# Optimization experiments

Hardware: AMD Instinct MI355X
Metric: run time of the kernel (lower is better)

The kernel has to match this reference:

```python
import jax, jax.numpy as jnp
import numpy as np

B, T, D = 1, 2048, 2048
H, HD = 32, 64
HEAD_COUNTS = np.array([8, 6, 4, 4, 6, 4])  # reasoning, creativity, curiosity, emotional, memory, meta
NEG = -1e9


def rope_tables(seq_len, dim, dtype):
    inv_freq = 1.0 / (10000.0 ** (jnp.arange(0, dim, 2, dtype=jnp.float32) / dim))
    t = jnp.arange(seq_len, dtype=jnp.float32)
    freqs = jnp.outer(t, inv_freq)            # [T, dim/2]
    emb = jnp.concatenate([freqs, freqs], -1) # [T, dim]
    return jnp.cos(emb).astype(dtype), jnp.sin(emb).astype(dtype)


def rotate_half(x):
    x1, x2 = jnp.split(x, 2, axis=-1)
    return jnp.concatenate([-x2, x1], axis=-1)


def setup_inputs() -> dict:
    key = jax.random.key(0)
    ks = jax.random.split(key, 8)
    x = jax.random.normal(ks[0], (B, T, D), jnp.float32)
    mask = jnp.tril(jnp.ones((T, T), jnp.int32))[None, None]  # causal [1,1,T,T]
    context_bias = jax.random.normal(ks[1], (B, T, T), jnp.float32) * 0.02
    mod_weights = jax.random.uniform(ks[2], (B, 6), jnp.float32, 0.5, 1.5)
    Wq = jax.random.normal(ks[3], (D, D), jnp.float32) * 0.02
    Wk = jax.random.normal(ks[4], (D, D), jnp.float32) * 0.02
    Wv = jax.random.normal(ks[5], (D, D), jnp.float32) * 0.02
    Wo = jax.random.normal(ks[6], (D, D), jnp.float32) * 0.02
    temp_scales = jnp.ones((H,), jnp.float32)
    return {"x": x, "mask": mask, "context_bias": context_bias,
            "mod_weights": mod_weights, "Wq": Wq, "Wk": Wk, "Wv": Wv,
            "Wo": Wo, "temp_scales": temp_scales}


def reference(x, mask, context_bias, mod_weights, Wq, Wk, Wv, Wo, temp_scales):
    b, t, d = x.shape
    # projections (torch Linear: y = x @ W.T)
    Q = (x @ Wq.T).reshape(b, t, H, HD).transpose(0, 2, 1, 3)  # [B,H,T,HD]
    K = (x @ Wk.T).reshape(b, t, H, HD).transpose(0, 2, 1, 3)
    V = (x @ Wv.T).reshape(b, t, H, HD).transpose(0, 2, 1, 3)
    cos, sin = rope_tables(t, HD, x.dtype)
    cos, sin = cos[None, None], sin[None, None]
    Q = Q * cos + rotate_half(Q) * sin
    K = K * cos + rotate_half(K) * sin
    scale = (HD ** -0.5) * temp_scales.reshape(1, H, 1, 1)
    attn = jnp.einsum('bhqd,bhkd->bhqk', Q, K) * scale
    attn = jnp.where(mask == 0, NEG, attn)
    attn = attn + context_bias[:, None]
    # per-head module reweight: expand [B,6] -> [B,H]
    w = jnp.repeat(mod_weights, np.asarray(HEAD_COUNTS), axis=1, total_repeat_length=H)
    attn = attn * w[:, :, None, None]
    attn = jax.nn.softmax(attn, axis=-1)
    out = jnp.einsum('bhqk,bhkd->bhqd', attn, V)
    out = out.transpose(0, 2, 1, 3).reshape(b, t, d)
    return out @ Wo.T
```

## Files before the change

kernel.cpp:

```cpp
#include <hip/hip_runtime.h>
#include <hip/hip_bf16.h>
#include <cstdint>
#include <cstddef>

typedef __bf16 bf16;
typedef bf16 bf16x4 __attribute__((ext_vector_type(4)));
typedef bf16 bf16x8 __attribute__((ext_vector_type(8)));
typedef float f32x4 __attribute__((ext_vector_type(4)));

#define MFMA_BF16(a,b,c) __builtin_amdgcn_mfma_f32_16x16x32_bf16((a),(b),(c),0,0,0)

typedef __attribute__((address_space(1))) const void gvoid;
typedef __attribute__((address_space(3))) void svoid;
__device__ __forceinline__ void gload16(const bf16* g, bf16* l){
  __builtin_amdgcn_global_load_lds((gvoid*)g, (svoid*)l, 16, 0, 0);
}

__device__ __forceinline__ int head_group(int h){
  return (h<8)?0:(h<14)?1:(h<18)?2:(h<22)?3:(h<28)?4:5;
}

struct CvtArgs { const float* src[5]; bf16* dst[5]; };
__global__ __launch_bounds__(256) void cvt5_kernel(CvtArgs a, int n){
  const int z = blockIdx.y;
  const float* __restrict__ in = a.src[z];
  bf16* __restrict__ out = a.dst[z];
  int i = (blockIdx.x*256 + threadIdx.x)*8;
  if (i >= n) return;
  const float4* p = (const float4*)(in + i);
  float4 va = p[0], vb = p[1];
  bf16x8 o;
  o[0]=(bf16)va.x; o[1]=(bf16)va.y; o[2]=(bf16)va.z; o[3]=(bf16)va.w;
  o[4]=(bf16)vb.x; o[5]=(bf16)vb.y; o[6]=(bf16)vb.z; o[7]=(bf16)vb.w;
  *(bf16x8*)(out+i) = o;
}

__global__ void rope_tab_kernel(float* __restrict__ cosT, float* __restrict__ sinT){
  int t = blockIdx.x, i = threadIdx.x;
  float invf = powf(10000.0f, -((float)i)/32.0f);
  float ang = (float)t * invf;
  cosT[t*32+i] = cosf(ang);
  sinT[t*32+i] = sinf(ang);
}

__device__ __forceinline__ void gemm_core(const bf16* __restrict__ A,
                                          const bf16* __restrict__ B,
                                          int row0, int col0,
                                          f32x4 (&acc)[4][4]){
  __shared__ bf16 As[128*32];
  __shared__ bf16 Bs[128*32];
  const int tid  = threadIdx.x;
  const int wave = tid>>6, lane = tid&63;
  const int l16  = lane&15, lg = lane>>4;
  const int wr   = wave>>1, wc = wave&1;

  const bf16* Ag0 = A + (size_t)(row0 + wave*32      + (lane>>2))*2048 + (lane&3)*8;
  const bf16* Ag1 = A + (size_t)(row0 + wave*32 + 16 + (lane>>2))*2048 + (lane&3)*8;
  const bf16* Bg0 = B + (size_t)(col0 + wave*32      + (lane>>2))*2048 + (lane&3)*8;
  const bf16* Bg1 = B + (size_t)(col0 + wave*32 + 16 + (lane>>2))*2048 + (lane&3)*8;
  bf16* AsB0 = As + (wave*32     )*32;
  bf16* AsB1 = As + (wave*32 + 16)*32;
  bf16* BsB0 = Bs + (wave*32     )*32;
  bf16* BsB1 = Bs + (wave*32 + 16)*32;

  #pragma unroll
  for (int m=0;m<4;++m)
    #pragma unroll
    for (int n=0;n<4;++n)
      #pragma unroll
      for (int r=0;r<4;++r) acc[m][n][r] = 0.f;

  for (int kt=0; kt<64; ++kt){
    const int ko = kt*32;
    gload16(Ag0 + ko, AsB0);
    gload16(Ag1 + ko, AsB1);
    gload16(Bg0 + ko, BsB0);
    gload16(Bg1 + ko, BsB1);
    __syncthreads();
    bf16x8 af[4], bfr[4];
    #pragma unroll
    for (int m=0;m<4;++m) af[m]  = *(const bf16x8*)&As[(wr*64+m*16+l16)*32 + lg*8];
    #pragma unroll
    for (int n=0;n<4;++n) bfr[n] = *(const bf16x8*)&Bs[(wc*64+n*16+l16)*32 + lg*8];
    #pragma unroll
    for (int m=0;m<4;++m)
      #pragma unroll
      for (int n=0;n<4;++n)
        acc[m][n] = MFMA_BF16(af[m], bfr[n], acc[m][n]);
    __syncthreads();
  }
}

__global__ __launch_bounds__(256) void gemm_qkv_kernel(
    const bf16* __restrict__ A,
    const bf16* __restrict__ B0, const bf16* __restrict__ B1, const bf16* __restrict__ B2,
    bf16* __restrict__ Qs, bf16* __restrict__ Ks, bf16* __restrict__ Vt,
    const float* __restrict__ cosT, const float* __restrict__ sinT,
    const float* __restrict__ mw, const float* __restrict__ ts){
  const int z = blockIdx.z;
  const bf16* B = (z==0)?B0:((z==1)?B1:B2);
  const int row0 = blockIdx.y*128, col0 = blockIdx.x*128;

  f32x4 acc[4][4];
  gemm_core(A, B, row0, col0, acc);

  const int tid  = threadIdx.x;
  const int wave = tid>>6, lane = tid&63;
  const int l16  = lane&15, lg = lane>>4;
  const int wr   = wave>>1, wc = wave&1;
  const int h    = (col0 + wc*64) >> 6;

  if (z == 2){
    #pragma unroll
    for (int n=0;n<4;++n){
      const int d = n*16 + l16;
      #pragma unroll
      for (int m=0;m<4;++m){
        const int t0 = row0 + wr*64 + m*16 + lg*4;
        bf16x4 v;
        #pragma unroll
        for (int r=0;r<4;++r) v[r] = (bf16)acc[m][n][r];
        *(bf16x4*)&Vt[((size_t)h*64 + d)*2048 + t0] = v;
      }
    }
  } else {
    const float sc = (z==0) ? 0.125f*ts[h]*mw[head_group(h)] : 1.0f;
    bf16* Out = (z==0) ? Qs : Ks;
    #pragma unroll
    for (int m=0;m<4;++m){
      #pragma unroll
      for (int r=0;r<4;++r){
        const int t = row0 + wr*64 + m*16 + lg*4 + r;
        const float* ct = cosT + t*32;
        const float* st = sinT + t*32;
        bf16* dst = Out + ((size_t)h*2048 + t)*64;
        #pragma unroll
        for (int n=0;n<2;++n){
          const int i = n*16 + l16;
          const float c = ct[i], s = st[i];
          const float a1 = acc[m][n][r], a2 = acc[m][n+2][r];
          dst[i]    = (bf16)((a1*c - a2*s)*sc);
          dst[i+32] = (bf16)((a2*c + a1*s)*sc);
        }
      }
    }
  }
}

__global__ __launch_bounds__(256) void gemm_out_kernel(
    const bf16* __restrict__ A, const bf16* __restrict__ B, float* __restrict__ C){
  const int row0 = blockIdx.y*128, col0 = blockIdx.x*128;
  f32x4 acc[4][4];
  gemm_core(A, B, row0, col0, acc);
  const int tid  = threadIdx.x;
  const int wave = tid>>6, lane = tid&63;
  const int l16  = lane&15, lg = lane>>4;
  const int wr   = wave>>1, wc = wave&1;
  #pragma unroll
  for (int m=0;m<4;++m)
    #pragma unroll
    for (int n=0;n<4;++n)
      #pragma unroll
      for (int r=0;r<4;++r){
        size_t idx = (size_t)(row0 + wr*64 + m*16 + lg*4 + r)*2048
                   + col0 + wc*64 + n*16 + l16;
        C[idx] = acc[m][n][r];
      }
}

__global__ __launch_bounds__(512) void attn_kernel(
    const bf16* __restrict__ Qs, const bf16* __restrict__ Ks,
    const bf16* __restrict__ Vt, const float* __restrict__ biasf,
    const float* __restrict__ mw, bf16* __restrict__ attout){
  const int n  = blockIdx.x;
  const int h  = ((n>>8)<<4) | ((n>>4)&15);
  const int qt = (n&256) ? (n&15) : 15-(n&15);
  const int tid = threadIdx.x, wid = tid>>6, lane = tid&63;
  const int l16 = lane&15, lg = lane>>4;
  const float w_h = mw[head_group(h)];
  const int qbase = qt*128 + wid*16;
  const int qg0 = qbase + lg*4;
  const int qtop = qbase + 15;
  const int nkt = 2*qt + 2;

  __shared__ bf16 Kl[2][4096];
  __shared__ bf16 Vl[2][4096];
  __shared__ bf16 plds[8][16][72];

  const int srow = tid>>3, ssub = tid&7;
  const bf16* Kg = Ks + (size_t)h*2048*64 + srow*64 + ssub*8;
  const bf16* Vg = Vt + ((size_t)h*64 + srow)*2048 + ssub*8;
  const int wsw = srow*64 + ((ssub ^ (srow&7))<<3);

  const bf16* Qp = Qs + ((size_t)h*2048 + qbase + l16)*64 + lg*8;
  bf16x8 qf0 = *(const bf16x8*)Qp;
  bf16x8 qf1 = *(const bf16x8*)(Qp + 32);

  const float* Bg = biasf + (size_t)qg0*2048;

  f32x4 O[4];
  float l[4] = {0.f,0.f,0.f,0.f};
  #pragma unroll
  for (int c=0;c<4;++c)
    #pragma unroll
    for (int r=0;r<4;++r) O[c][r] = 0.f;

  int rK0[4], rK1[4];
  #pragma unroll
  for (int c=0;c<4;++c){
    const int row = c*16 + l16;
    rK0[c] = row*64 + (((lg  ) ^ (row&7))<<3);
    rK1[c] = row*64 + (((4+lg) ^ (row&7))<<3);
  }

  {
    bf16x8 k0v = *(const bf16x8*)Kg;
    bf16x8 v0v = *(const bf16x8*)Vg;
    *(bf16x8*)&Kl[0][wsw] = k0v;
    *(bf16x8*)&Vl[0][wsw] = v0v;
  }
  __syncthreads();

  int cur = 0;
  for (int kt=0; kt<nkt; ++kt){
    const int k0 = kt*64;
    const bool more = (kt+1 < nkt);
    bf16x8 kA, vA;
    if (more){
      kA = *(const bf16x8*)(Kg + (size_t)(k0+64)*64);
      vA = *(const bf16x8*)(Vg + (k0+64));
    }

    if (k0 <= qtop){
      float bv[4][4];
      #pragma unroll
      for (int c=0;c<4;++c)
        #pragma unroll
        for (int r=0;r<4;++r)
          bv[c][r] = Bg[(size_t)r*2048 + k0 + c*16 + l16];

      f32x4 S[4];
      #pragma unroll
      for (int c=0;c<4;++c)
        #pragma unroll
        for (int r=0;r<4;++r) S[c][r] = 0.f;
      #pragma unroll
      for (int c=0;c<4;++c){
        bf16x8 kf0 = *(const bf16x8*)&Kl[cur][rK0[c]];
        bf16x8 kf1 = *(const bf16x8*)&Kl[cur][rK1[c]];
        S[c] = MFMA_BF16(qf0, kf0, S[c]);
        S[c] = MFMA_BF16(qf1, kf1, S[c]);
      }

      #pragma unroll
      for (int c=0;c<4;++c){
        const int kg = k0 + c*16 + l16;
        #pragma unroll
        for (int r=0;r<4;++r){
          float s = S[c][r] + w_h*bv[c][r];
          if (kg > qg0+r) s = -1e30f;
          const float p = __expf(s - 4.0f);
          S[c][r] = p; l[r] += p;
        }
      }

      #pragma unroll
      for (int c=0;c<4;++c)
        #pragma unroll
        for (int r=0;r<4;++r)
          plds[wid][lg*4+r][c*16+l16] = (bf16)S[c][r];
      bf16x8 pf0 = *(const bf16x8*)&plds[wid][l16][lg*8];
      bf16x8 pf1 = *(const bf16x8*)&plds[wid][l16][lg*8+32];

      #pragma unroll
      for (int c=0;c<4;++c){
        bf16x8 vf0 = *(const bf16x8*)&Vl[cur][rK0[c]];
        bf16x8 vf1 = *(const bf16x8*)&Vl[cur][rK1[c]];
        O[c] = MFMA_BF16(pf0, vf0, O[c]);
        O[c] = MFMA_BF16(pf1, vf1, O[c]);
      }
    }

    if (more){
      *(bf16x8*)&Kl[cur^1][wsw] = kA;
      *(bf16x8*)&Vl[cur^1][wsw] = vA;
    }
    __syncthreads();
    cur ^= (int)more;
  }

  #pragma unroll
  for (int r=0;r<4;++r){
    float v = l[r];
    v += __shfl_xor(v,1);
    v += __shfl_xor(v,2);
    v += __shfl_xor(v,4);
    v += __shfl_xor(v,8);
    l[r] = 1.0f / v;
  }
  #pragma unroll
  for (int c=0;c<4;++c)
    #pragma unroll
    for (int r=0;r<4;++r)
      attout[(size_t)(qg0+r)*2048 + h*64 + c*16 + l16] = (bf16)(O[c][r]*l[r]);
}

extern "C" void kernel_launch(void* const* d_in, const int* in_sizes, int n_in,
                              void* d_out, int out_size, void* d_ws, size_t ws_size,
                              hipStream_t stream){
  const float* x    = (const float*)d_in[0];
  const float* bias = (const float*)d_in[2];
  const float* mw   = (const float*)d_in[3];
  const float* Wq   = (const float*)d_in[4];
  const float* Wk   = (const float*)d_in[5];
  const float* Wv   = (const float*)d_in[6];
  const float* Wo   = (const float*)d_in[7];
  const float* ts   = (const float*)d_in[8];
  float* out = (float*)d_out;

  const size_t SZ = (size_t)2048*2048;
  bf16* base = (bf16*)d_ws;
  bf16* xb   = base;
  bf16* Wqb  = base + 1*SZ;
  bf16* Wkb  = base + 2*SZ;
  bf16* Wvb  = base + 3*SZ;
  bf16* Wob  = base + 4*SZ;
  bf16* Qsb  = base + 5*SZ;
  bf16* Ksb  = base + 6*SZ;
  bf16* Vtb  = base + 7*SZ;
  bf16* att  = base + 8*SZ;
  float* cosT = (float*)(base + 9*SZ);
  float* sinT = cosT + 2048*32;

  CvtArgs ca;
  ca.src[0]=x;  ca.src[1]=Wq;  ca.src[2]=Wk;  ca.src[3]=Wv;  ca.src[4]=Wo;
  ca.dst[0]=xb; ca.dst[1]=Wqb; ca.dst[2]=Wkb; ca.dst[3]=Wvb; ca.dst[4]=Wob;
  const int nb = (int)(SZ/8/256);
  cvt5_kernel<<<dim3(nb,5),256,0,stream>>>(ca, (int)SZ);
  rope_tab_kernel<<<2048,32,0,stream>>>(cosT, sinT);
  gemm_qkv_kernel<<<dim3(16,16,3),256,0,stream>>>(xb, Wqb,Wkb,Wvb,
                                                  Qsb,Ksb,Vtb, cosT,sinT, mw,ts);
  attn_kernel<<<512,512,0,stream>>>(Qsb,Ksb,Vtb,bias,mw,att);
  gemm_out_kernel<<<dim3(16,16),256,0,stream>>>(att, Wob, out);
}
```

Measured before the change: 181.6 us.

## Give each attention wave two query sub-tiles to reuse K/V fragments

The attention kernel moves from 8 waves of 16 query rows to 4 waves of 32 rows. Each K/V fragment read from LDS now feeds two MFMAs, halving the LDS fragment traffic per query row, and each thread now loads two 16-byte chunks of K/V per tile. It also seeds the S accumulators with the weighted bias, applies the causal mask only on diagonal tiles, and repacks the rope table kernel into 256-thread blocks. In exchange there are fewer waves per block and more registers per thread, which may lower occupancy and latency hiding.

```diff
diff --git a/kernel.cpp b/kernel.cpp
--- a/kernel.cpp
+++ b/kernel.cpp
@@ -35,8 +35,10 @@
   *(bf16x8*)(out+i) = o;
 }
 
-__global__ void rope_tab_kernel(float* __restrict__ cosT, float* __restrict__ sinT){
-  int t = blockIdx.x, i = threadIdx.x;
+__global__ __launch_bounds__(256) void rope_tab_kernel(float* __restrict__ cosT,
+                                                       float* __restrict__ sinT){
+  const int t = blockIdx.x*8 + (threadIdx.x>>5);
+  const int i = threadIdx.x&31;
   float invf = powf(10000.0f, -((float)i)/32.0f);
   float ang = (float)t * invf;
   cosT[t*32+i] = cosf(ang);
@@ -168,7 +170,7 @@
       }
 }
 
-__global__ __launch_bounds__(512) void attn_kernel(
+__global__ __launch_bounds__(256) void attn_kernel(
     const bf16* __restrict__ Qs, const bf16* __restrict__ Ks,
     const bf16* __restrict__ Vt, const float* __restrict__ biasf,
     const float* __restrict__ mw, bf16* __restrict__ attout){
@@ -178,32 +180,40 @@
   const int tid = threadIdx.x, wid = tid>>6, lane = tid&63;
   const int l16 = lane&15, lg = lane>>4;
   const float w_h = mw[head_group(h)];
-  const int qbase = qt*128 + wid*16;
-  const int qg0 = qbase + lg*4;
-  const int qtop = qbase + 15;
-  const int nkt = 2*qt + 2;
+  const int qw   = qt*128 + wid*32;
+  const int qtop = qw + 31;
+  const int nkt  = 2*qt + 2;
 
   __shared__ bf16 Kl[2][4096];
   __shared__ bf16 Vl[2][4096];
-  __shared__ bf16 plds[8][16][72];
-
-  const int srow = tid>>3, ssub = tid&7;
+  __shared__ bf16 plds[4][32][68];
+
+  const int srow = tid>>2, ssub = (tid&3)*2;
   const bf16* Kg = Ks + (size_t)h*2048*64 + srow*64 + ssub*8;
   const bf16* Vg = Vt + ((size_t)h*64 + srow)*2048 + ssub*8;
-  const int wsw = srow*64 + ((ssub ^ (srow&7))<<3);
-
-  const bf16* Qp = Qs + ((size_t)h*2048 + qbase + l16)*64 + lg*8;
-  bf16x8 qf0 = *(const bf16x8*)Qp;
-  bf16x8 qf1 = *(const bf16x8*)(Qp + 32);
-
-  const float* Bg = biasf + (size_t)qg0*2048;
-
-  f32x4 O[4];
-  float l[4] = {0.f,0.f,0.f,0.f};
-  #pragma unroll
-  for (int c=0;c<4;++c)
-    #pragma unroll
-    for (int r=0;r<4;++r) O[c][r] = 0.f;
+  const int wsw0 = srow*64 + (((ssub  ) ^ (srow&7))<<3);
+  const int wsw1 = srow*64 + (((ssub+1) ^ (srow&7))<<3);
+
+  bf16x8 qf[2][2];
+  #pragma unroll
+  for (int m=0;m<2;++m){
+    const bf16* Qp = Qs + ((size_t)h*2048 + qw + m*16 + l16)*64 + lg*8;
+    qf[m][0] = *(const bf16x8*)Qp;
+    qf[m][1] = *(const bf16x8*)(Qp + 32);
+  }
+
+  const float* Bg = biasf + (size_t)(qw + lg*4)*2048;
+
+  f32x4 O[2][4];
+  float l[2][4];
+  #pragma unroll
+  for (int m=0;m<2;++m)
+    #pragma unroll
+    for (int c=0;c<4;++c){
+      #pragma unroll
+      for (int r=0;r<4;++r) O[m][c][r] = 0.f;
+      l[m][c] = 0.f;
+    }
 
   int rK0[4], rK1[4];
   #pragma unroll
@@ -214,10 +224,12 @@
   }
 
   {
-    bf16x8 k0v = *(const bf16x8*)Kg;
-    bf16x8 v0v = *(const bf16x8*)Vg;
-    *(bf16x8*)&Kl[0][wsw] = k0v;
-    *(bf16x8*)&Vl[0][wsw] = v0v;
+    bf16x8 k0a = *(const bf16x8*)Kg;
+    bf16x8 k0b = *(const bf16x8*)(Kg + 8);
+    bf16x8 v0a = *(const bf16x8*)Vg;
+    bf16x8 v0b = *(const bf16x8*)(Vg + 8);
+    *(bf16x8*)&Kl[0][wsw0] = k0a;  *(bf16x8*)&Kl[0][wsw1] = k0b;
+    *(bf16x8*)&Vl[0][wsw0] = v0a;  *(bf16x8*)&Vl[0][wsw1] = v0b;
   }
   __syncthreads();
 
@@ -225,84 +237,114 @@
   for (int kt=0; kt<nkt; ++kt){
     const int k0 = kt*64;
     const bool more = (kt+1 < nkt);
-    bf16x8 kA, vA;
+    bf16x8 kA, kB, vA, vB;
     if (more){
-      kA = *(const bf16x8*)(Kg + (size_t)(k0+64)*64);
-      vA = *(const bf16x8*)(Vg + (k0+64));
+      const bf16* Kn = Kg + (size_t)(k0+64)*64;
+      const bf16* Vn = Vg + (k0+64);
+      kA = *(const bf16x8*)Kn;  kB = *(const bf16x8*)(Kn + 8);
+      vA = *(const bf16x8*)Vn;  vB = *(const bf16x8*)(Vn + 8);
     }
 
     if (k0 <= qtop){
-      float bv[4][4];
-      #pragma unroll
-      for (int c=0;c<4;++c)
-        #pragma unroll
-        for (int r=0;r<4;++r)
-          bv[c][r] = Bg[(size_t)r*2048 + k0 + c*16 + l16];
-
-      f32x4 S[4];
-      #pragma unroll
-      for (int c=0;c<4;++c)
-        #pragma unroll
-        for (int r=0;r<4;++r) S[c][r] = 0.f;
+      f32x4 S[2][4];
+      #pragma unroll
+      for (int m=0;m<2;++m)
+        #pragma unroll
+        for (int c=0;c<4;++c)
+          #pragma unroll
+          for (int r=0;r<4;++r)
+            S[m][c][r] = w_h * Bg[(size_t)(m*16+r)*2048 + k0 + c*16 + l16];
+
       #pragma unroll
       for (int c=0;c<4;++c){
         bf16x8 kf0 = *(const bf16x8*)&Kl[cur][rK0[c]];
         bf16x8 kf1 = *(const bf16x8*)&Kl[cur][rK1[c]];
-        S[c] = MFMA_BF16(qf0, kf0, S[c]);
-        S[c] = MFMA_BF16(qf1, kf1, S[c]);
-      }
-
-      #pragma unroll
-      for (int c=0;c<4;++c){
-        const int kg = k0 + c*16 + l16;
-        #pragma unroll
-        for (int r=0;r<4;++r){
-          float s = S[c][r] + w_h*bv[c][r];
-          if (kg > qg0+r) s = -1e30f;
-          const float p = __expf(s - 4.0f);
-          S[c][r] = p; l[r] += p;
+        #pragma unroll
+        for (int m=0;m<2;++m){
+          S[m][c] = MFMA_BF16(qf[m][0], kf0, S[m][c]);
+          S[m][c] = MFMA_BF16(qf[m][1], kf1, S[m][c]);
         }
       }
 
-      #pragma unroll
-      for (int c=0;c<4;++c)
-        #pragma unroll
-        for (int r=0;r<4;++r)
-          plds[wid][lg*4+r][c*16+l16] = (bf16)S[c][r];
-      bf16x8 pf0 = *(const bf16x8*)&plds[wid][l16][lg*8];
-      bf16x8 pf1 = *(const bf16x8*)&plds[wid][l16][lg*8+32];
+      if (k0 + 63 > qw){
+        #pragma unroll
+        for (int m=0;m<2;++m)
+          #pragma unroll
+          for (int c=0;c<4;++c){
+            const int kg = k0 + c*16 + l16;
+            const int qg = qw + m*16 + lg*4;
+            #pragma unroll
+            for (int r=0;r<4;++r){
+              float p = __expf(S[m][c][r] - 4.0f);
+              if (kg > qg + r) p = 0.f;
+              S[m][c][r] = p; l[m][r] += p;
+            }
+          }
+      } else {
+        #pragma unroll
+        for (int m=0;m<2;++m)
+          #pragma unroll
+          for (int c=0;c<4;++c)
+            #pragma unroll
+            for (int r=0;r<4;++r){
+              const float p = __expf(S[m][c][r] - 4.0f);
+              S[m][c][r] = p; l[m][r] += p;
+            }
+      }
+
+      #pragma unroll
+      for (int m=0;m<2;++m)
+        #pragma unroll
+        for (int c=0;c<4;++c)
+          #pragma unroll
+          for (int r=0;r<4;++r)
+            plds[wid][m*16+lg*4+r][c*16+l16] = (bf16)S[m][c][r];
+      bf16x8 pf[2][2];
+      #pragma unroll
+      for (int m=0;m<2;++m){
+        pf[m][0] = *(const bf16x8*)&plds[wid][m*16+l16][lg*8];
+        pf[m][1] = *(const bf16x8*)&plds[wid][m*16+l16][32+lg*8];
+      }
 
       #pragma unroll
       for (int c=0;c<4;++c){
         bf16x8 vf0 = *(const bf16x8*)&Vl[cur][rK0[c]];
         bf16x8 vf1 = *(const bf16x8*)&Vl[cur][rK1[c]];
-        O[c] = MFMA_BF16(pf0, vf0, O[c]);
-        O[c] = MFMA_BF16(pf1, vf1, O[c]);
+        #pragma unroll
+        for (int m=0;m<2;++m){
+          O[m][c] = MFMA_BF16(pf[m][0], vf0, O[m][c]);
+          O[m][c] = MFMA_BF16(pf[m][1], vf1, O[m][c]);
+        }
       }
     }
 
     if (more){
-      *(bf16x8*)&Kl[cur^1][wsw] = kA;
-      *(bf16x8*)&Vl[cur^1][wsw] = vA;
+      *(bf16x8*)&Kl[cur^1][wsw0] = kA;  *(bf16x8*)&Kl[cur^1][wsw1] = kB;
+      *(bf16x8*)&Vl[cur^1][wsw0] = vA;  *(bf16x8*)&Vl[cur^1][wsw1] = vB;
     }
     __syncthreads();
     cur ^= (int)more;
   }
 
   #pragma unroll
-  for (int r=0;r<4;++r){
-    float v = l[r];
-    v += __shfl_xor(v,1);
-    v += __shfl_xor(v,2);
-    v += __shfl_xor(v,4);
-    v += __shfl_xor(v,8);
-    l[r] = 1.0f / v;
-  }
-  #pragma unroll
-  for (int c=0;c<4;++c)
-    #pragma unroll
-    for (int r=0;r<4;++r)
-      attout[(size_t)(qg0+r)*2048 + h*64 + c*16 + l16] = (bf16)(O[c][r]*l[r]);
+  for (int m=0;m<2;++m)
+    #pragma unroll
+    for (int r=0;r<4;++r){
+      float v = l[m][r];
+      v += __shfl_xor(v,1);
+      v += __shfl_xor(v,2);
+      v += __shfl_xor(v,4);
+      v += __shfl_xor(v,8);
+      l[m][r] = 1.0f / v;
+    }
+  #pragma unroll
+  for (int m=0;m<2;++m)
+    #pragma unroll
+    for (int c=0;c<4;++c)
+      #pragma unroll
+      for (int r=0;r<4;++r)
+        attout[(size_t)(qw + m*16 + lg*4 + r)*2048 + h*64 + c*16 + l16]
+          = (bf16)(O[m][c][r]*l[m][r]);
 }
 
 extern "C" void kernel_launch(void* const* d_in, const int* in_sizes, int n_in,
@@ -337,9 +379,9 @@
   ca.dst[0]=xb; ca.dst[1]=Wqb; ca.dst[2]=Wkb; ca.dst[3]=Wvb; ca.dst[4]=Wob;
   const int nb = (int)(SZ/8/256);
   cvt5_kernel<<<dim3(nb,5),256,0,stream>>>(ca, (int)SZ);
-  rope_tab_kernel<<<2048,32,0,stream>>>(cosT, sinT);
+  rope_tab_kernel<<<256,256,0,stream>>>(cosT, sinT);
   gemm_qkv_kernel<<<dim3(16,16,3),256,0,stream>>>(xb, Wqb,Wkb,Wvb,
                                                   Qsb,Ksb,Vtb, cosT,sinT, mw,ts);
-  attn_kernel<<<512,512,0,stream>>>(Qsb,Ksb,Vtb,bias,mw,att);
+  attn_kernel<<<512,256,0,stream>>>(Qsb,Ksb,Vtb,bias,mw,att);
   gemm_out_kernel<<<dim3(16,16),256,0,stream>>>(att, Wob, out);
 }
```

Result: slower. 217.5 us (+19.8%).

## Prefetch bf16 context bias a tile ahead and raise MFMA wave priority

Applied to the files above, without the earlier changes.

Converts the fp32 context bias to bf16 in the batch conversion kernel and prefetches the next tile's pre-scaled bias into registers one iteration ahead. The bias is then used as the initial MFMA accumulator instead of being added afterwards. It also wraps the MFMA blocks in s_setprio and gives the rope table kernel larger blocks. The goal is to halve bias traffic and hide its load latency behind compute. The costs are an extra conversion pass over a 2048x2048 array, more registers per thread, and bf16 rounding of the bias.

```diff
diff --git a/kernel.cpp b/kernel.cpp
--- a/kernel.cpp
+++ b/kernel.cpp
@@ -20,8 +20,8 @@
   return (h<8)?0:(h<14)?1:(h<18)?2:(h<22)?3:(h<28)?4:5;
 }
 
-struct CvtArgs { const float* src[5]; bf16* dst[5]; };
-__global__ __launch_bounds__(256) void cvt5_kernel(CvtArgs a, int n){
+struct CvtArgs { const float* src[6]; bf16* dst[6]; };
+__global__ __launch_bounds__(256) void cvt6_kernel(CvtArgs a, int n){
   const int z = blockIdx.y;
   const float* __restrict__ in = a.src[z];
   bf16* __restrict__ out = a.dst[z];
@@ -35,8 +35,10 @@
   *(bf16x8*)(out+i) = o;
 }
 
-__global__ void rope_tab_kernel(float* __restrict__ cosT, float* __restrict__ sinT){
-  int t = blockIdx.x, i = threadIdx.x;
+__global__ __launch_bounds__(256) void rope_tab_kernel(float* __restrict__ cosT,
+                                                       float* __restrict__ sinT){
+  const int t = blockIdx.x*8 + (threadIdx.x>>5);
+  const int i = threadIdx.x&31;
   float invf = powf(10000.0f, -((float)i)/32.0f);
   float ang = (float)t * invf;
   cosT[t*32+i] = cosf(ang);
@@ -170,7 +172,7 @@
 
 __global__ __launch_bounds__(512) void attn_kernel(
     const bf16* __restrict__ Qs, const bf16* __restrict__ Ks,
-    const bf16* __restrict__ Vt, const float* __restrict__ biasf,
+    const bf16* __restrict__ Vt, const bf16* __restrict__ biasb,
     const float* __restrict__ mw, bf16* __restrict__ attout){
   const int n  = blockIdx.x;
   const int h  = ((n>>8)<<4) | ((n>>4)&15);
@@ -196,7 +198,7 @@
   bf16x8 qf0 = *(const bf16x8*)Qp;
   bf16x8 qf1 = *(const bf16x8*)(Qp + 32);
 
-  const float* Bg = biasf + (size_t)qg0*2048;
+  const bf16* Bg = biasb + (size_t)qg0*2048;
 
   f32x4 O[4];
   float l[4] = {0.f,0.f,0.f,0.f};
@@ -212,6 +214,13 @@
     rK0[c] = row*64 + (((lg  ) ^ (row&7))<<3);
     rK1[c] = row*64 + (((4+lg) ^ (row&7))<<3);
   }
+
+  float bc[4][4];
+  #pragma unroll
+  for (int c=0;c<4;++c)
+    #pragma unroll
+    for (int r=0;r<4;++r)
+      bc[c][r] = w_h * (float)Bg[(size_t)r*2048 + c*16 + l16];
 
   {
     bf16x8 k0v = *(const bf16x8*)Kg;
@@ -226,24 +235,25 @@
     const int k0 = kt*64;
     const bool more = (kt+1 < nkt);
     bf16x8 kA, vA;
+    float bn[4][4];
     if (more){
       kA = *(const bf16x8*)(Kg + (size_t)(k0+64)*64);
       vA = *(const bf16x8*)(Vg + (k0+64));
+      #pragma unroll
+      for (int c=0;c<4;++c)
+        #pragma unroll
+        for (int r=0;r<4;++r)
+          bn[c][r] = w_h * (float)Bg[(size_t)r*2048 + (k0+64) + c*16 + l16];
     }
 
     if (k0 <= qtop){
-      float bv[4][4];
+      f32x4 S[4];
       #pragma unroll
       for (int c=0;c<4;++c)
         #pragma unroll
-        for (int r=0;r<4;++r)
-          bv[c][r] = Bg[(size_t)r*2048 + k0 + c*16 + l16];
-
-      f32x4 S[4];
-      #pragma unroll
-      for (int c=0;c<4;++c)
-        #pragma unroll
-        for (int r=0;r<4;++r) S[c][r] = 0.f;
+        for (int r=0;r<4;++r) S[c][r] = bc[c][r];
+
+      __builtin_amdgcn_s_setprio(1);
       #pragma unroll
       for (int c=0;c<4;++c){
         bf16x8 kf0 = *(const bf16x8*)&Kl[cur][rK0[c]];
@@ -251,13 +261,14 @@
         S[c] = MFMA_BF16(qf0, kf0, S[c]);
         S[c] = MFMA_BF16(qf1, kf1, S[c]);
       }
+      __builtin_amdgcn_s_setprio(0);
 
       #pragma unroll
       for (int c=0;c<4;++c){
         const int kg = k0 + c*16 + l16;
         #pragma unroll
         for (int r=0;r<4;++r){
-          float s = S[c][r] + w_h*bv[c][r];
+          float s = S[c][r];
           if (kg > qg0+r) s = -1e30f;
           const float p = __expf(s - 4.0f);
           S[c][r] = p; l[r] += p;
@@ -272,6 +283,7 @@
       bf16x8 pf0 = *(const bf16x8*)&plds[wid][l16][lg*8];
       bf16x8 pf1 = *(const bf16x8*)&plds[wid][l16][lg*8+32];
 
+      __builtin_amdgcn_s_setprio(1);
       #pragma unroll
       for (int c=0;c<4;++c){
         bf16x8 vf0 = *(const bf16x8*)&Vl[cur][rK0[c]];
@@ -279,11 +291,16 @@
         O[c] = MFMA_BF16(pf0, vf0, O[c]);
         O[c] = MFMA_BF16(pf1, vf1, O[c]);
       }
+      __builtin_amdgcn_s_setprio(0);
     }
 
     if (more){
       *(bf16x8*)&Kl[cur^1][wsw] = kA;
       *(bf16x8*)&Vl[cur^1][wsw] = vA;
+      #pragma unroll
+      for (int c=0;c<4;++c)
+        #pragma unroll
+        for (int r=0;r<4;++r) bc[c][r] = bn[c][r];
     }
     __syncthreads();
     cur ^= (int)more;
@@ -325,21 +342,22 @@
   bf16* Wkb  = base + 2*SZ;
   bf16* Wvb  = base + 3*SZ;
   bf16* Wob  = base + 4*SZ;
-  bf16* Qsb  = base + 5*SZ;
-  bf16* Ksb  = base + 6*SZ;
-  bf16* Vtb  = base + 7*SZ;
-  bf16* att  = base + 8*SZ;
-  float* cosT = (float*)(base + 9*SZ);
+  bf16* bb   = base + 5*SZ;
+  bf16* Qsb  = base + 6*SZ;
+  bf16* Ksb  = base + 7*SZ;
+  bf16* Vtb  = base + 8*SZ;
+  bf16* att  = base + 9*SZ;
+  float* cosT = (float*)(base + 10*SZ);
   float* sinT = cosT + 2048*32;
 
   CvtArgs ca;
-  ca.src[0]=x;  ca.src[1]=Wq;  ca.src[2]=Wk;  ca.src[3]=Wv;  ca.src[4]=Wo;
-  ca.dst[0]=xb; ca.dst[1]=Wqb; ca.dst[2]=Wkb; ca.dst[3]=Wvb; ca.dst[4]=Wob;
+  ca.src[0]=x;  ca.src[1]=Wq;  ca.src[2]=Wk;  ca.src[3]=Wv;  ca.src[4]=Wo;  ca.src[5]=bias;
+  ca.dst[0]=xb; ca.dst[1]=Wqb; ca.dst[2]=Wkb; ca.dst[3]=Wvb; ca.dst[4]=Wob; ca.dst[5]=bb;
   const int nb = (int)(SZ/8/256);
-  cvt5_kernel<<<dim3(nb,5),256,0,stream>>>(ca, (int)SZ);
-  rope_tab_kernel<<<2048,32,0,stream>>>(cosT, sinT);
+  cvt6_kernel<<<dim3(nb,6),256,0,stream>>>(ca, (int)SZ);
+  rope_tab_kernel<<<256,256,0,stream>>>(cosT, sinT);
   gemm_qkv_kernel<<<dim3(16,16,3),256,0,stream>>>(xb, Wqb,Wkb,Wvb,
                                                   Qsb,Ksb,Vtb, cosT,sinT, mw,ts);
-  attn_kernel<<<512,512,0,stream>>>(Qsb,Ksb,Vtb,bias,mw,att);
+  attn_kernel<<<512,512,0,stream>>>(Qsb,Ksb,Vtb,bb,mw,att);
   gemm_out_kernel<<<dim3(16,16),256,0,stream>>>(att, Wob, out);
 }
```

New measurement: 180.4 us. No clear change (-0.7%).
